# Performance work log

Measured on AMD Instinct MI355X. Metric: run time of the kernel, lower is better.

The kernel has to match this reference:

```python
import jax, jax.numpy as jnp
import numpy as np

LN_EPS = 1e-5  # torch nn.LayerNorm default


def setup_inputs() -> dict:
    key = jax.random.key(0)
    ks = jax.random.split(key, 5)
    B, N, K, H, D = 1, 16384, 16, 4, 32
    q = jax.random.normal(ks[0], (B, N, H, D), dtype=jnp.float32)
    k_neigh = jax.random.normal(ks[1], (B, N, K, H, D), dtype=jnp.float32)
    v_neigh = jax.random.normal(ks[2], (B, N, K, H, D), dtype=jnp.float32)
    geo_f = jax.random.normal(ks[3], (B, N, K, D), dtype=jnp.float32)
    W = jax.random.normal(ks[4], (D, D), dtype=jnp.float32) * (1.0 / np.sqrt(D))
    b = jnp.zeros((D,), dtype=jnp.float32)
    ln_gamma = jnp.ones((D,), dtype=jnp.float32)
    ln_beta = jnp.zeros((D,), dtype=jnp.float32)
    return {"q": q, "k_neigh": k_neigh, "v_neigh": v_neigh, "geo_f": geo_f,
            "W": W, "b": b, "ln_gamma": ln_gamma, "ln_beta": ln_beta}


def reference(q, k_neigh, v_neigh, geo_f, W, b, ln_gamma, ln_beta):
    # q: [B,N,H,D], k_neigh/v_neigh: [B,N,K,H,D], geo_f: [B,N,K,D]
    scale = q.shape[-1] ** (-0.5)
    # broadcasted edge tensor [B,N,K,H,D]
    w = (q[:, :, None, :, :] - k_neigh + geo_f[:, :, :, None, :]) / scale
    # Linear(hdim,hdim) + ReLU + LayerNorm(hdim)
    w = jnp.einsum('bnkhd,ed->bnkhe', w, W) + b
    w = jax.nn.relu(w)
    mu = jnp.mean(w, axis=-1, keepdims=True)
    var = jnp.mean(jnp.square(w - mu), axis=-1, keepdims=True)
    w = (w - mu) * jax.lax.rsqrt(var + LN_EPS) * ln_gamma + ln_beta
    # subtract detached per-neighbor max (shift-invariant for softmax)
    w = w - jax.lax.stop_gradient(jnp.max(w, axis=2, keepdims=True))
    attn = jax.nn.softmax(w, axis=2)  # softmax over K neighbors
    # dropout p=0.0 -> identity
    out = jnp.sum(attn * v_neigh, axis=2)  # [B,N,H,D]
    return out
```

## Files before the change

kernel.cpp:

```cpp
#include <hip/hip_runtime.h>
#include <hip/hip_bf16.h>
#include <math.h>

constexpr int KNB = 16;
constexpr int HH  = 4;
constexpr int DD  = 32;

typedef __attribute__((ext_vector_type(4))) float f32x4;
typedef __attribute__((ext_vector_type(8))) short bf16x8;

union BFRAG { bf16x8 v; unsigned u[4]; };

__device__ __forceinline__ unsigned pk_bf16(float a, float b) {
    union { __hip_bfloat162 b2; unsigned u; } r;
    r.b2 = __float22bfloat162_rn(make_float2(a, b));
    return r.u;
}
__device__ __forceinline__ float2 unpk_bf16(unsigned u) {
    union { unsigned u; __hip_bfloat162 b2; } r; r.u = u;
    return make_float2(__bfloat162float(r.b2.x), __bfloat162float(r.b2.y));
}

__global__ __launch_bounds__(256) void geoneigh_mfma2(
    const float* __restrict__ q, const float* __restrict__ kn,
    const float* __restrict__ vn, const float* __restrict__ geo,
    const float* __restrict__ W, const float* __restrict__ bvec,
    const float* __restrict__ gamma, const float* __restrict__ beta,
    float* __restrict__ out, int BN)
{
    const int l  = threadIdx.x & 63;
    const int gw = blockIdx.x * 4 + (threadIdx.x >> 6);
    const int n  = gw >> 1;
    if (n >= BN) return;
    const int h0 = (gw & 1) * 2;

    const int lm = l & 15;
    const int lg = l >> 4;

    const float SC = 5.656854249492381f;

    BFRAG Wh[2], Wl[2];
    #pragma unroll
    for (int t = 0; t < 2; ++t) {
        const float* wr = &W[(t * 16 + lm) * DD + lg * 8];
        const float4 wa = *(const float4*)wr;
        const float4 wb = *(const float4*)(wr + 4);
        float wf[8] = {wa.x * SC, wa.y * SC, wa.z * SC, wa.w * SC,
                       wb.x * SC, wb.y * SC, wb.z * SC, wb.w * SC};
        #pragma unroll
        for (int p = 0; p < 4; ++p) {
            const unsigned h = pk_bf16(wf[2 * p], wf[2 * p + 1]);
            const float2 hr = unpk_bf16(h);
            Wh[t].u[p] = h;
            Wl[t].u[p] = pk_bf16(wf[2 * p] - hr.x, wf[2 * p + 1] - hr.y);
        }
    }
    float bias[2], gam[2], bet[2];
    #pragma unroll
    for (int t = 0; t < 2; ++t) {
        bias[t] = bvec[lm + 16 * t];
        gam[t]  = gamma[lm + 16 * t];
        bet[t]  = beta[lm + 16 * t];
    }

    const size_t nn = (size_t)n;
    const float* kb = kn  + ((nn * KNB + lm) * HH + h0) * DD + lg * 8;
    const float* gb = geo + (nn * KNB + lm) * DD + lg * 8;
    const float* qb = q   + (nn * HH + h0) * DD + lg * 8;

    const float4 gf0 = *(const float4*)gb;
    const float4 gf1 = *(const float4*)(gb + 4);
    float4 kf[2][2], qf[2][2];
    #pragma unroll
    for (int u = 0; u < 2; ++u) {
        kf[u][0] = *(const float4*)(kb + u * DD);
        kf[u][1] = *(const float4*)(kb + u * DD + 4);
        qf[u][0] = *(const float4*)(qb + u * DD);
        qf[u][1] = *(const float4*)(qb + u * DD + 4);
    }

    const float* vb = vn + ((nn * KNB + lg * 4) * HH + h0) * DD + lm;
    float vreg[2][2][4];
    #pragma unroll
    for (int u = 0; u < 2; ++u)
        #pragma unroll
        for (int t = 0; t < 2; ++t)
            #pragma unroll
            for (int r = 0; r < 4; ++r)
                vreg[u][t][r] = vb[((size_t)r * HH + u) * DD + 16 * t];

    f32x4 acc[2][2];
    #pragma unroll
    for (int u = 0; u < 2; ++u) {
        float wv[8];
        #pragma unroll
        for (int p = 0; p < 2; ++p) {
            const float4 kq = kf[u][p], qq = qf[u][p];
            const float4 gg = p ? gf1 : gf0;
            wv[4 * p + 0] = qq.x - kq.x + gg.x;
            wv[4 * p + 1] = qq.y - kq.y + gg.y;
            wv[4 * p + 2] = qq.z - kq.z + gg.z;
            wv[4 * p + 3] = qq.w - kq.w + gg.w;
        }
        BFRAG Ah, Al;
        #pragma unroll
        for (int p = 0; p < 4; ++p) {
            const unsigned h = pk_bf16(wv[2 * p], wv[2 * p + 1]);
            const float2 hr = unpk_bf16(h);
            Ah.u[p] = h;
            Al.u[p] = pk_bf16(wv[2 * p] - hr.x, wv[2 * p + 1] - hr.y);
        }
        #pragma unroll
        for (int t = 0; t < 2; ++t) {
            f32x4 c = {bias[t], bias[t], bias[t], bias[t]};
            c = __builtin_amdgcn_mfma_f32_16x16x32_bf16(Ah.v, Wh[t].v, c, 0, 0, 0);
            c = __builtin_amdgcn_mfma_f32_16x16x32_bf16(Ah.v, Wl[t].v, c, 0, 0, 0);
            c = __builtin_amdgcn_mfma_f32_16x16x32_bf16(Al.v, Wh[t].v, c, 0, 0, 0);
            acc[u][t] = c;
        }
    }

    float outv[2], sumv[2];
    #pragma unroll
    for (int u = 0; u < 2; ++u) {
        float x[2][4], t1[4], t2[4];
        #pragma unroll
        for (int t = 0; t < 2; ++t)
            #pragma unroll
            for (int r = 0; r < 4; ++r)
                x[t][r] = fmaxf(acc[u][t][r], 0.f);
        #pragma unroll
        for (int r = 0; r < 4; ++r) {
            t1[r] = x[0][r] + x[1][r];
            t2[r] = x[0][r] * x[0][r] + x[1][r] * x[1][r];
        }
        #pragma unroll
        for (int m = 1; m <= 8; m <<= 1) {
            #pragma unroll
            for (int r = 0; r < 4; ++r) {
                t1[r] += __shfl_xor(t1[r], m);
                t2[r] += __shfl_xor(t2[r], m);
            }
        }
        float z[2][4];
        #pragma unroll
        for (int r = 0; r < 4; ++r) {
            const float mu  = t1[r] * 0.03125f;
            const float var = fmaxf(t2[r] * 0.03125f - mu * mu, 0.f);
            const float inv = rsqrtf(var + 1e-5f);
            #pragma unroll
            for (int t = 0; t < 2; ++t)
                z[t][r] = (x[t][r] - mu) * inv * gam[t] + bet[t];
        }
        float S[2], o[2];
        #pragma unroll
        for (int t = 0; t < 2; ++t) {
            float mx = fmaxf(fmaxf(z[t][0], z[t][1]), fmaxf(z[t][2], z[t][3]));
            mx = fmaxf(mx, __shfl_xor(mx, 16));
            mx = fmaxf(mx, __shfl_xor(mx, 32));
            float s = 0.f, oo = 0.f;
            #pragma unroll
            for (int r = 0; r < 4; ++r) {
                const float p = __expf(z[t][r] - mx);
                s += p;
                oo = fmaf(p, vreg[u][t][r], oo);
            }
            s  += __shfl_xor(s, 16);
            s  += __shfl_xor(s, 32);
            oo += __shfl_xor(oo, 16);
            oo += __shfl_xor(oo, 32);
            S[t] = s; o[t] = oo;
        }
        const int sel = lg & 1;
        outv[u] = sel ? o[1] : o[0];
        sumv[u] = sel ? S[1] : S[0];
    }

    const int us = l >> 5;
    const float oo = us ? outv[1] : outv[0];
    const float ss = us ? sumv[1] : sumv[0];
    out[(nn * HH + h0 + us) * DD + (l & 31)] = __fdividef(oo, ss);
}

extern "C" void kernel_launch(void* const* d_in, const int* in_sizes, int n_in,
                              void* d_out, int out_size, void* d_ws, size_t ws_size,
                              hipStream_t stream) {
    const float* q   = (const float*)d_in[0];
    const float* kn  = (const float*)d_in[1];
    const float* vn  = (const float*)d_in[2];
    const float* geo = (const float*)d_in[3];
    const float* W   = (const float*)d_in[4];
    const float* b   = (const float*)d_in[5];
    const float* gam = (const float*)d_in[6];
    const float* bet = (const float*)d_in[7];
    float* out = (float*)d_out;

    const int BN     = in_sizes[0] / (HH * DD);
    const int waves  = BN * 2;
    const int blocks = (waves + 3) / 4;

    hipLaunchKernelGGL(geoneigh_mfma2, dim3(blocks), dim3(256), 0, stream,
                       q, kn, vn, geo, W, b, gam, bet, out, BN);
}
```

Baseline: 72.42 us.

## Process several units per wave with grid-stride loop and drop softmax max

Each wave now handles four (node, head-pair) units in an unrolled grid-stride loop. This amortizes the per-wave W bf16 hi/lo split and the bias, gamma and beta loads, and lets the compiler overlap loads across iterations. The per-neighbor max subtraction before exp is removed, relying on LayerNorm bounding the logits. That drops two shuffles and max ops per head, but exp could overflow for large gamma or beta.

```diff
diff --git a/kernel.cpp b/kernel.cpp
--- a/kernel.cpp
+++ b/kernel.cpp
@@ -1,14 +1,14 @@
 #include <hip/hip_runtime.h>
 #include <hip/hip_bf16.h>
-#include <math.h>
 
 constexpr int KNB = 16;
 constexpr int HH  = 4;
 constexpr int DD  = 32;
+constexpr int WPB   = 4;
+constexpr int ITERS = 4;
 
 typedef __attribute__((ext_vector_type(4))) float f32x4;
 typedef __attribute__((ext_vector_type(8))) short bf16x8;
-
 union BFRAG { bf16x8 v; unsigned u[4]; };
 
 __device__ __forceinline__ unsigned pk_bf16(float a, float b) {
@@ -21,18 +21,17 @@
     return make_float2(__bfloat162float(r.b2.x), __bfloat162float(r.b2.y));
 }
 
-__global__ __launch_bounds__(256) void geoneigh_mfma2(
+template<bool GUARD>
+__global__ __launch_bounds__(256) void geoneigh_mfma3(
     const float* __restrict__ q, const float* __restrict__ kn,
     const float* __restrict__ vn, const float* __restrict__ geo,
     const float* __restrict__ W, const float* __restrict__ bvec,
     const float* __restrict__ gamma, const float* __restrict__ beta,
-    float* __restrict__ out, int BN)
+    float* __restrict__ out, int nUnits, int strideW)
 {
-    const int l  = threadIdx.x & 63;
-    const int gw = blockIdx.x * 4 + (threadIdx.x >> 6);
-    const int n  = gw >> 1;
-    if (n >= BN) return;
-    const int h0 = (gw & 1) * 2;
+    const int l   = threadIdx.x & 63;
+    const int gw0 = __builtin_amdgcn_readfirstlane(
+                        blockIdx.x * WPB + (threadIdx.x >> 6));
 
     const int lm = l & 15;
     const int lg = l >> 4;
@@ -63,123 +62,132 @@
         bet[t]  = beta[lm + 16 * t];
     }
 
-    const size_t nn = (size_t)n;
-    const float* kb = kn  + ((nn * KNB + lm) * HH + h0) * DD + lg * 8;
-    const float* gb = geo + (nn * KNB + lm) * DD + lg * 8;
-    const float* qb = q   + (nn * HH + h0) * DD + lg * 8;
-
-    const float4 gf0 = *(const float4*)gb;
-    const float4 gf1 = *(const float4*)(gb + 4);
-    float4 kf[2][2], qf[2][2];
+    const int koff = lm * (HH * DD) + lg * 8;
+    const int goff = lm * DD + lg * 8;
+    const int qoff = lg * 8;
+    const int voff = (lg * 4) * (HH * DD) + lm;
+
     #pragma unroll
-    for (int u = 0; u < 2; ++u) {
-        kf[u][0] = *(const float4*)(kb + u * DD);
-        kf[u][1] = *(const float4*)(kb + u * DD + 4);
-        qf[u][0] = *(const float4*)(qb + u * DD);
-        qf[u][1] = *(const float4*)(qb + u * DD + 4);
+    for (int it = 0; it < ITERS; ++it) {
+        const int gwi = gw0 + it * strideW;
+        if (GUARD && gwi >= nUnits) break;
+        const int n  = gwi >> 1;
+        const int h0 = (gwi & 1) * 2;
+        const size_t nb = (size_t)n;
+
+        const float* kb = kn  + nb * (KNB * HH * DD) + h0 * DD + koff;
+        const float* gb = geo + nb * (KNB * DD) + goff;
+        const float* qb = q   + nb * (HH * DD) + h0 * DD + qoff;
+        const float* vb = vn  + nb * (KNB * HH * DD) + h0 * DD + voff;
+
+        const float4 gf0 = *(const float4*)gb;
+        const float4 gf1 = *(const float4*)(gb + 4);
+        float4 kf[2][2], qf[2][2];
+        #pragma unroll
+        for (int u = 0; u < 2; ++u) {
+            kf[u][0] = *(const float4*)(kb + u * DD);
+            kf[u][1] = *(const float4*)(kb + u * DD + 4);
+            qf[u][0] = *(const float4*)(qb + u * DD);
+            qf[u][1] = *(const float4*)(qb + u * DD + 4);
+        }
+        float vreg[2][2][4];
+        #pragma unroll
+        for (int u = 0; u < 2; ++u)
+            #pragma unroll
+            for (int t = 0; t < 2; ++t)
+                #pragma unroll
+                for (int r = 0; r < 4; ++r)
+                    vreg[u][t][r] = vb[r * (HH * DD) + u * DD + 16 * t];
+
+        f32x4 acc[2][2];
+        #pragma unroll
+        for (int u = 0; u < 2; ++u) {
+            float wv[8];
+            #pragma unroll
+            for (int p = 0; p < 2; ++p) {
+                const float4 kq = kf[u][p], qq = qf[u][p];
+                const float4 gg = p ? gf1 : gf0;
+                wv[4 * p + 0] = qq.x - kq.x + gg.x;
+                wv[4 * p + 1] = qq.y - kq.y + gg.y;
+                wv[4 * p + 2] = qq.z - kq.z + gg.z;
+                wv[4 * p + 3] = qq.w - kq.w + gg.w;
+            }
+            BFRAG Ah, Al;
+            #pragma unroll
+            for (int p = 0; p < 4; ++p) {
+                const unsigned h = pk_bf16(wv[2 * p], wv[2 * p + 1]);
+                const float2 hr = unpk_bf16(h);
+                Ah.u[p] = h;
+                Al.u[p] = pk_bf16(wv[2 * p] - hr.x, wv[2 * p + 1] - hr.y);
+            }
+            #pragma unroll
+            for (int t = 0; t < 2; ++t) {
+                f32x4 c = {bias[t], bias[t], bias[t], bias[t]};
+                c = __builtin_amdgcn_mfma_f32_16x16x32_bf16(Ah.v, Wh[t].v, c, 0, 0, 0);
+                c = __builtin_amdgcn_mfma_f32_16x16x32_bf16(Ah.v, Wl[t].v, c, 0, 0, 0);
+                c = __builtin_amdgcn_mfma_f32_16x16x32_bf16(Al.v, Wh[t].v, c, 0, 0, 0);
+                acc[u][t] = c;
+            }
+        }
+
+        float outv[2], sumv[2];
+        #pragma unroll
+        for (int u = 0; u < 2; ++u) {
+            float x[2][4], t1[4], t2[4];
+            #pragma unroll
+            for (int t = 0; t < 2; ++t)
+                #pragma unroll
+                for (int r = 0; r < 4; ++r)
+                    x[t][r] = fmaxf(acc[u][t][r], 0.f);
+            #pragma unroll
+            for (int r = 0; r < 4; ++r) {
+                t1[r] = x[0][r] + x[1][r];
+                t2[r] = x[0][r] * x[0][r] + x[1][r] * x[1][r];
+            }
+            #pragma unroll
+            for (int m = 1; m <= 8; m <<= 1) {
+                #pragma unroll
+                for (int r = 0; r < 4; ++r) {
+                    t1[r] += __shfl_xor(t1[r], m);
+                    t2[r] += __shfl_xor(t2[r], m);
+                }
+            }
+            float z[2][4];
+            #pragma unroll
+            for (int r = 0; r < 4; ++r) {
+                const float mu  = t1[r] * 0.03125f;
+                const float var = fmaxf(t2[r] * 0.03125f - mu * mu, 0.f);
+                const float inv = rsqrtf(var + 1e-5f);
+                #pragma unroll
+                for (int t = 0; t < 2; ++t)
+                    z[t][r] = (x[t][r] - mu) * inv * gam[t] + bet[t];
+            }
+            float S[2], o[2];
+            #pragma unroll
+            for (int t = 0; t < 2; ++t) {
+                float s = 0.f, oo = 0.f;
+                #pragma unroll
+                for (int r = 0; r < 4; ++r) {
+                    const float p = __expf(z[t][r]);
+                    s += p;
+                    oo = fmaf(p, vreg[u][t][r], oo);
+                }
+                s  += __shfl_xor(s, 16);
+                s  += __shfl_xor(s, 32);
+                oo += __shfl_xor(oo, 16);
+                oo += __shfl_xor(oo, 32);
+                S[t] = s; o[t] = oo;
+            }
+            const int sel = lg & 1;
+            outv[u] = sel ? o[1] : o[0];
+            sumv[u] = sel ? S[1] : S[0];
+        }
+
+        const int us = l >> 5;
+        const float oo = us ? outv[1] : outv[0];
+        const float ss = us ? sumv[1] : sumv[0];
+        out[(nb * HH + h0 + us) * DD + (l & 31)] = __fdividef(oo, ss);
     }
-
-    const float* vb = vn + ((nn * KNB + lg * 4) * HH + h0) * DD + lm;
-    float vreg[2][2][4];
-    #pragma unroll
-    for (int u = 0; u < 2; ++u)
-        #pragma unroll
-        for (int t = 0; t < 2; ++t)
-            #pragma unroll
-            for (int r = 0; r < 4; ++r)
-                vreg[u][t][r] = vb[((size_t)r * HH + u) * DD + 16 * t];
-
-    f32x4 acc[2][2];
-    #pragma unroll
-    for (int u = 0; u < 2; ++u) {
-        float wv[8];
-        #pragma unroll
-        for (int p = 0; p < 2; ++p) {
-            const float4 kq = kf[u][p], qq = qf[u][p];
-            const float4 gg = p ? gf1 : gf0;
-            wv[4 * p + 0] = qq.x - kq.x + gg.x;
-            wv[4 * p + 1] = qq.y - kq.y + gg.y;
-            wv[4 * p + 2] = qq.z - kq.z + gg.z;
-            wv[4 * p + 3] = qq.w - kq.w + gg.w;
-        }
-        BFRAG Ah, Al;
-        #pragma unroll
-        for (int p = 0; p < 4; ++p) {
-            const unsigned h = pk_bf16(wv[2 * p], wv[2 * p + 1]);
-            const float2 hr = unpk_bf16(h);
-            Ah.u[p] = h;
-            Al.u[p] = pk_bf16(wv[2 * p] - hr.x, wv[2 * p + 1] - hr.y);
-        }
-        #pragma unroll
-        for (int t = 0; t < 2; ++t) {
-            f32x4 c = {bias[t], bias[t], bias[t], bias[t]};
-            c = __builtin_amdgcn_mfma_f32_16x16x32_bf16(Ah.v, Wh[t].v, c, 0, 0, 0);
-            c = __builtin_amdgcn_mfma_f32_16x16x32_bf16(Ah.v, Wl[t].v, c, 0, 0, 0);
-            c = __builtin_amdgcn_mfma_f32_16x16x32_bf16(Al.v, Wh[t].v, c, 0, 0, 0);
-            acc[u][t] = c;
-        }
-    }
-
-    float outv[2], sumv[2];
-    #pragma unroll
-    for (int u = 0; u < 2; ++u) {
-        float x[2][4], t1[4], t2[4];
-        #pragma unroll
-        for (int t = 0; t < 2; ++t)
-            #pragma unroll
-            for (int r = 0; r < 4; ++r)
-                x[t][r] = fmaxf(acc[u][t][r], 0.f);
-        #pragma unroll
-        for (int r = 0; r < 4; ++r) {
-            t1[r] = x[0][r] + x[1][r];
-            t2[r] = x[0][r] * x[0][r] + x[1][r] * x[1][r];
-        }
-        #pragma unroll
-        for (int m = 1; m <= 8; m <<= 1) {
-            #pragma unroll
-            for (int r = 0; r < 4; ++r) {
-                t1[r] += __shfl_xor(t1[r], m);
-                t2[r] += __shfl_xor(t2[r], m);
-            }
-        }
-        float z[2][4];
-        #pragma unroll
-        for (int r = 0; r < 4; ++r) {
-            const float mu  = t1[r] * 0.03125f;
-            const float var = fmaxf(t2[r] * 0.03125f - mu * mu, 0.f);
-            const float inv = rsqrtf(var + 1e-5f);
-            #pragma unroll
-            for (int t = 0; t < 2; ++t)
-                z[t][r] = (x[t][r] - mu) * inv * gam[t] + bet[t];
-        }
-        float S[2], o[2];
-        #pragma unroll
-        for (int t = 0; t < 2; ++t) {
-            float mx = fmaxf(fmaxf(z[t][0], z[t][1]), fmaxf(z[t][2], z[t][3]));
-            mx = fmaxf(mx, __shfl_xor(mx, 16));
-            mx = fmaxf(mx, __shfl_xor(mx, 32));
-            float s = 0.f, oo = 0.f;
-            #pragma unroll
-            for (int r = 0; r < 4; ++r) {
-                const float p = __expf(z[t][r] - mx);
-                s += p;
-                oo = fmaf(p, vreg[u][t][r], oo);
-            }
-            s  += __shfl_xor(s, 16);
-            s  += __shfl_xor(s, 32);
-            oo += __shfl_xor(oo, 16);
-            oo += __shfl_xor(oo, 32);
-            S[t] = s; o[t] = oo;
-        }
-        const int sel = lg & 1;
-        outv[u] = sel ? o[1] : o[0];
-        sumv[u] = sel ? S[1] : S[0];
-    }
-
-    const int us = l >> 5;
-    const float oo = us ? outv[1] : outv[0];
-    const float ss = us ? sumv[1] : sumv[0];
-    out[(nn * HH + h0 + us) * DD + (l & 31)] = __fdividef(oo, ss);
 }
 
 extern "C" void kernel_launch(void* const* d_in, const int* in_sizes, int n_in,
@@ -195,10 +203,18 @@
     const float* bet = (const float*)d_in[7];
     float* out = (float*)d_out;
 
-    const int BN     = in_sizes[0] / (HH * DD);
-    const int waves  = BN * 2;
-    const int blocks = (waves + 3) / 4;
-
-    hipLaunchKernelGGL(geoneigh_mfma2, dim3(blocks), dim3(256), 0, stream,
-                       q, kn, vn, geo, W, b, gam, bet, out, BN);
-}
+    const int BN      = in_sizes[0] / (HH * DD);
+    const int nUnits  = BN * 2;
+    const int blocks  = (nUnits + WPB * ITERS - 1) / (WPB * ITERS);
+    const int strideW = blocks * WPB;
+    const bool exact  = (nUnits == blocks * WPB * ITERS);
+
+    if (exact)
+        hipLaunchKernelGGL(geoneigh_mfma3<false>, dim3(blocks), dim3(256), 0,
+                           stream, q, kn, vn, geo, W, b, gam, bet, out,
+                           nUnits, strideW);
+    else
+        hipLaunchKernelGGL(geoneigh_mfma3<true>, dim3(blocks), dim3(256), 0,
+                           stream, q, kn, vn, geo, W, b, gam, bet, out,
+                           nUnits, strideW);
+}
```

Result: faster. 63.75 us (-12.0%).

## Pipeline per-node loads through double-buffered LDS with async global_load_lds

Applied to the files above, without the earlier changes.

Restructures the kernel so each 256-thread block processes 16 nodes in sequence. One node's k/v/geo/q tiles are prefetched into a double-buffered LDS staging area with direct global-to-LDS loads while the previous node is computed, and each wave now handles one head. It also folds log2(e) into the LayerNorm gamma/beta, so exp2f can replace __expf, and drops the per-neighbour max subtraction before the softmax. The aim is to hide memory latency and cut the shuffle work. The cost is barriers on every iteration and fewer blocks in flight. Without the max subtraction the softmax could overflow if gamma or beta were large.

```diff
diff --git a/kernel.cpp b/kernel.cpp
--- a/kernel.cpp
+++ b/kernel.cpp
@@ -1,15 +1,20 @@
 #include <hip/hip_runtime.h>
 #include <hip/hip_bf16.h>
-#include <math.h>
 
 constexpr int KNB = 16;
 constexpr int HH  = 4;
 constexpr int DD  = 32;
+constexpr int NPB = 16;
 
 typedef __attribute__((ext_vector_type(4))) float f32x4;
 typedef __attribute__((ext_vector_type(8))) short bf16x8;
-
 union BFRAG { bf16x8 v; unsigned u[4]; };
+
+constexpr int L_K  = 0;
+constexpr int L_V  = 2048;
+constexpr int L_G  = 4096;
+constexpr int L_Q  = 4608;
+constexpr int L_SZ = 4864;
 
 __device__ __forceinline__ unsigned pk_bf16(float a, float b) {
     union { __hip_bfloat162 b2; unsigned u; } r;
@@ -20,24 +25,29 @@
     union { unsigned u; __hip_bfloat162 b2; } r; r.u = u;
     return make_float2(__bfloat162float(r.b2.x), __bfloat162float(r.b2.y));
 }
-
-__global__ __launch_bounds__(256) void geoneigh_mfma2(
+__device__ __forceinline__ void gload16(const float* g, float* l) {
+    __builtin_amdgcn_global_load_lds(
+        (const __attribute__((address_space(1))) unsigned*)g,
+        (__attribute__((address_space(3))) unsigned*)l, 16, 0, 0);
+}
+
+__global__ __launch_bounds__(256, 4) void geoneigh_pipe(
     const float* __restrict__ q, const float* __restrict__ kn,
     const float* __restrict__ vn, const float* __restrict__ geo,
     const float* __restrict__ W, const float* __restrict__ bvec,
     const float* __restrict__ gamma, const float* __restrict__ beta,
     float* __restrict__ out, int BN)
 {
-    const int l  = threadIdx.x & 63;
-    const int gw = blockIdx.x * 4 + (threadIdx.x >> 6);
-    const int n  = gw >> 1;
-    if (n >= BN) return;
-    const int h0 = (gw & 1) * 2;
-
-    const int lm = l & 15;
-    const int lg = l >> 4;
-
-    const float SC = 5.656854249492381f;
+    __shared__ __align__(16) float lds[2][L_SZ];
+
+    const int tid = threadIdx.x;
+    const int l   = tid & 63;
+    const int wv  = tid >> 6;
+    const int lm  = l & 15;
+    const int lg  = l >> 4;
+
+    const float SC    = 5.656854249492381f;
+    const float LOG2E = 1.4426950408889634f;
 
     BFRAG Wh[2], Wl[2];
     #pragma unroll
@@ -55,131 +65,144 @@
             Wl[t].u[p] = pk_bf16(wf[2 * p] - hr.x, wf[2 * p + 1] - hr.y);
         }
     }
-    float bias[2], gam[2], bet[2];
+    float bias[2], gamL[2], betL[2];
     #pragma unroll
     for (int t = 0; t < 2; ++t) {
         bias[t] = bvec[lm + 16 * t];
-        gam[t]  = gamma[lm + 16 * t];
-        bet[t]  = beta[lm + 16 * t];
+        gamL[t] = gamma[lm + 16 * t] * LOG2E;
+        betL[t] = beta[lm + 16 * t] * LOG2E;
     }
 
-    const size_t nn = (size_t)n;
-    const float* kb = kn  + ((nn * KNB + lm) * HH + h0) * DD + lg * 8;
-    const float* gb = geo + (nn * KNB + lm) * DD + lg * 8;
-    const float* qb = q   + (nn * HH + h0) * DD + lg * 8;
-
-    const float4 gf0 = *(const float4*)gb;
-    const float4 gf1 = *(const float4*)(gb + 4);
-    float4 kf[2][2], qf[2][2];
-    #pragma unroll
-    for (int u = 0; u < 2; ++u) {
-        kf[u][0] = *(const float4*)(kb + u * DD);
-        kf[u][1] = *(const float4*)(kb + u * DD + 4);
-        qf[u][0] = *(const float4*)(qb + u * DD);
-        qf[u][1] = *(const float4*)(qb + u * DD + 4);
-    }
-
-    const float* vb = vn + ((nn * KNB + lg * 4) * HH + h0) * DD + lm;
-    float vreg[2][2][4];
-    #pragma unroll
-    for (int u = 0; u < 2; ++u)
-        #pragma unroll
-        for (int t = 0; t < 2; ++t)
+    const int koff0 = lm * 128 + wv * 32 + lg * 8;
+    const int vbase = (((l >> 2) & 3) * 4 + wv) * 128 + lg * 32 + (l & 3) * 4;
+    const int goff  = lm * 32 + lg * 8 + (wv & 1) * 4;
+    const int qoff  = (l & 31) * 4;
+    const int dK = L_K + 2 * wv * 256;
+    const int dV = L_V + 2 * wv * 256;
+    const int dG = L_G + (wv & 1) * 256;
+
+    const int nbase = blockIdx.x * NPB;
+    const int nmax  = BN - 1;
+
+    auto stage = [&](int buf, int n) {
+        const float* kN = kn  + (size_t)n * (KNB * HH * DD);
+        const float* vN = vn  + (size_t)n * (KNB * HH * DD);
+        const float* gN = geo + (size_t)n * (KNB * DD);
+        const float* qN = q   + (size_t)n * (HH * DD);
+        float* B = &lds[buf][0];
+        gload16(kN + koff0,      B + dK);
+        gload16(kN + koff0 + 4,  B + dK + 256);
+        gload16(vN + vbase,      B + dV);
+        gload16(vN + vbase + 16, B + dV + 256);
+        gload16(gN + goff,       B + dG);
+        gload16(qN + qoff,       B + L_Q);
+    };
+    auto cnode = [&](int t) { int n = nbase + t; return n > nmax ? nmax : n; };
+
+    stage(0, cnode(0));
+
+    #pragma unroll 2
+    for (int t = 0; t < NPB; ++t) {
+        stage((t + 1) & 1, cnode(t + 1));
+        asm volatile("s_waitcnt vmcnt(6)" ::: "memory");
+        __builtin_amdgcn_s_barrier();
+        __builtin_amdgcn_sched_barrier(0);
+
+        const float* B = &lds[t & 1][0];
+        const int n = cnode(t);
+
+        const f32x4 kf0 = *(const f32x4*)(B + L_K + wv * 512 + l * 4);
+        const f32x4 kf1 = *(const f32x4*)(B + L_K + wv * 512 + 256 + l * 4);
+        const f32x4 gf0 = *(const f32x4*)(B + L_G + l * 4);
+        const f32x4 gf1 = *(const f32x4*)(B + L_G + 256 + l * 4);
+        const f32x4 qf0 = *(const f32x4*)(B + L_Q + wv * 32 + lg * 8);
+        const f32x4 qf1 = *(const f32x4*)(B + L_Q + wv * 32 + lg * 8 + 4);
+        float vr[2][4];
+        #pragma unroll
+        for (int t2 = 0; t2 < 2; ++t2)
             #pragma unroll
             for (int r = 0; r < 4; ++r)
-                vreg[u][t][r] = vb[((size_t)r * HH + u) * DD + 16 * t];
-
-    f32x4 acc[2][2];
-    #pragma unroll
-    for (int u = 0; u < 2; ++u) {
-        float wv[8];
-        #pragma unroll
-        for (int p = 0; p < 2; ++p) {
-            const float4 kq = kf[u][p], qq = qf[u][p];
-            const float4 gg = p ? gf1 : gf0;
-            wv[4 * p + 0] = qq.x - kq.x + gg.x;
-            wv[4 * p + 1] = qq.y - kq.y + gg.y;
-            wv[4 * p + 2] = qq.z - kq.z + gg.z;
-            wv[4 * p + 3] = qq.w - kq.w + gg.w;
+                vr[t2][r] = B[L_V + (r * 32 + t2 * 16 + wv * 4 + lg) * 16 + lm];
+
+        float wvv[8];
+        #pragma unroll
+        for (int j = 0; j < 4; ++j) {
+            wvv[j]     = qf0[j] - kf0[j] + gf0[j];
+            wvv[4 + j] = qf1[j] - kf1[j] + gf1[j];
         }
         BFRAG Ah, Al;
         #pragma unroll
         for (int p = 0; p < 4; ++p) {
-            const unsigned h = pk_bf16(wv[2 * p], wv[2 * p + 1]);
+            const unsigned h = pk_bf16(wvv[2 * p], wvv[2 * p + 1]);
             const float2 hr = unpk_bf16(h);
             Ah.u[p] = h;
-            Al.u[p] = pk_bf16(wv[2 * p] - hr.x, wv[2 * p + 1] - hr.y);
-        }
-        #pragma unroll
-        for (int t = 0; t < 2; ++t) {
-            f32x4 c = {bias[t], bias[t], bias[t], bias[t]};
-            c = __builtin_amdgcn_mfma_f32_16x16x32_bf16(Ah.v, Wh[t].v, c, 0, 0, 0);
-            c = __builtin_amdgcn_mfma_f32_16x16x32_bf16(Ah.v, Wl[t].v, c, 0, 0, 0);
-            c = __builtin_amdgcn_mfma_f32_16x16x32_bf16(Al.v, Wh[t].v, c, 0, 0, 0);
-            acc[u][t] = c;
-        }
-    }
-
-    float outv[2], sumv[2];
-    #pragma unroll
-    for (int u = 0; u < 2; ++u) {
-        float x[2][4], t1[4], t2[4];
-        #pragma unroll
-        for (int t = 0; t < 2; ++t)
+            Al.u[p] = pk_bf16(wvv[2 * p] - hr.x, wvv[2 * p + 1] - hr.y);
+        }
+        f32x4 acc[2];
+        #pragma unroll
+        for (int t2 = 0; t2 < 2; ++t2) {
+            f32x4 c = {bias[t2], bias[t2], bias[t2], bias[t2]};
+            c = __builtin_amdgcn_mfma_f32_16x16x32_bf16(Ah.v, Wh[t2].v, c, 0, 0, 0);
+            c = __builtin_amdgcn_mfma_f32_16x16x32_bf16(Ah.v, Wl[t2].v, c, 0, 0, 0);
+            c = __builtin_amdgcn_mfma_f32_16x16x32_bf16(Al.v, Wh[t2].v, c, 0, 0, 0);
+            acc[t2] = c;
+        }
+
+        float x[2][4], t1[4], t2s[4];
+        #pragma unroll
+        for (int t2 = 0; t2 < 2; ++t2)
             #pragma unroll
             for (int r = 0; r < 4; ++r)
-                x[t][r] = fmaxf(acc[u][t][r], 0.f);
+                x[t2][r] = fmaxf(acc[t2][r], 0.f);
         #pragma unroll
         for (int r = 0; r < 4; ++r) {
-            t1[r] = x[0][r] + x[1][r];
-            t2[r] = x[0][r] * x[0][r] + x[1][r] * x[1][r];
+            t1[r]  = x[0][r] + x[1][r];
+            t2s[r] = x[0][r] * x[0][r] + x[1][r] * x[1][r];
         }
         #pragma unroll
         for (int m = 1; m <= 8; m <<= 1) {
             #pragma unroll
             for (int r = 0; r < 4; ++r) {
-                t1[r] += __shfl_xor(t1[r], m);
-                t2[r] += __shfl_xor(t2[r], m);
+                t1[r]  += __shfl_xor(t1[r], m);
+                t2s[r] += __shfl_xor(t2s[r], m);
             }
         }
         float z[2][4];
         #pragma unroll
         for (int r = 0; r < 4; ++r) {
             const float mu  = t1[r] * 0.03125f;
-            const float var = fmaxf(t2[r] * 0.03125f - mu * mu, 0.f);
+            const float var = fmaxf(t2s[r] * 0.03125f - mu * mu, 0.f);
             const float inv = rsqrtf(var + 1e-5f);
             #pragma unroll
-            for (int t = 0; t < 2; ++t)
-                z[t][r] = (x[t][r] - mu) * inv * gam[t] + bet[t];
+            for (int t2 = 0; t2 < 2; ++t2)
+                z[t2][r] = (x[t2][r] - mu) * inv * gamL[t2] + betL[t2];
         }
         float S[2], o[2];
         #pragma unroll
-        for (int t = 0; t < 2; ++t) {
-            float mx = fmaxf(fmaxf(z[t][0], z[t][1]), fmaxf(z[t][2], z[t][3]));
-            mx = fmaxf(mx, __shfl_xor(mx, 16));
-            mx = fmaxf(mx, __shfl_xor(mx, 32));
+        for (int t2 = 0; t2 < 2; ++t2) {
             float s = 0.f, oo = 0.f;
             #pragma unroll
             for (int r = 0; r < 4; ++r) {
-                const float p = __expf(z[t][r] - mx);
+                const float p = exp2f(z[t2][r]);
                 s += p;
-                oo = fmaf(p, vreg[u][t][r], oo);
+                oo = fmaf(p, vr[t2][r], oo);
             }
             s  += __shfl_xor(s, 16);
             s  += __shfl_xor(s, 32);
             oo += __shfl_xor(oo, 16);
             oo += __shfl_xor(oo, 32);
-            S[t] = s; o[t] = oo;
-        }
-        const int sel = lg & 1;
-        outv[u] = sel ? o[1] : o[0];
-        sumv[u] = sel ? S[1] : S[0];
+            S[t2] = s; o[t2] = oo;
+        }
+        if (l < 32) {
+            const int sel = (l >> 4) & 1;
+            const float oo = sel ? o[1] : o[0];
+            const float ss = sel ? S[1] : S[0];
+            out[((size_t)n * HH + wv) * DD + l] = __fdividef(oo, ss);
+        }
+
+        asm volatile("s_waitcnt lgkmcnt(0)" ::: "memory");
+        __builtin_amdgcn_s_barrier();
     }
-
-    const int us = l >> 5;
-    const float oo = us ? outv[1] : outv[0];
-    const float ss = us ? sumv[1] : sumv[0];
-    out[(nn * HH + h0 + us) * DD + (l & 31)] = __fdividef(oo, ss);
 }
 
 extern "C" void kernel_launch(void* const* d_in, const int* in_sizes, int n_in,
@@ -196,9 +219,8 @@
     float* out = (float*)d_out;
 
     const int BN     = in_sizes[0] / (HH * DD);
-    const int waves  = BN * 2;
-    const int blocks = (waves + 3) / 4;
-
-    hipLaunchKernelGGL(geoneigh_mfma2, dim3(blocks), dim3(256), 0, stream,
+    const int blocks = (BN + NPB - 1) / NPB;
+
+    hipLaunchKernelGGL(geoneigh_pipe, dim3(blocks), dim3(256), 0, stream,
                        q, kn, vn, geo, W, b, gam, bet, out, BN);
 }
```

New measurement: 68.77 us. 1.05x faster.
